# Optimization experiments

Hardware: AMD Instinct MI355X
Metric: run time of the kernel (lower is better)

Reference implementation:

```python
import jax, jax.numpy as jnp
import numpy as np

B, C, H, W = 2, 64, 512, 512
HEADS = 4
EPS = 1e-12  # F.normalize eps


def setup_inputs() -> dict:
    key = jax.random.key(0)
    ks = jax.random.split(key, 7)
    s = 0.02
    return {
        "x": jax.random.normal(ks[0], (B, C, H, W), jnp.float32),
        "Wq": jax.random.normal(ks[1], (C, C), jnp.float32) * s,
        "Wk": jax.random.normal(ks[2], (C, C), jnp.float32) * s,
        "Wv": jax.random.normal(ks[3], (C, C), jnp.float32) * s,
        "Wp": jax.random.normal(ks[4], (C, C), jnp.float32) * s,
        "bp": jax.random.normal(ks[5], (C,), jnp.float32) * s,
        "rescale": jnp.ones((HEADS, 1, 1), jnp.float32),
    }


def reference(x, Wq, Wk, Wv, Wp, bp, rescale):
    b, c, h, w = x.shape
    n = h * w
    d = c // HEADS
    xf = x.reshape(b, c, n)  # 1x1 conv == channel matmul on flattened spatial

    def conv1x1(Wt):
        return jnp.einsum('oc,bcn->bon', Wt, xf)

    # torch: permute->reshape(b,n,c)->split heads->transpose == reshape conv out to (b,heads,d,n)
    q = conv1x1(Wq).reshape(b, HEADS, d, n)
    k = conv1x1(Wk).reshape(b, HEADS, d, n)
    v = conv1x1(Wv).reshape(b, HEADS, d, n)

    def l2norm(t):  # F.normalize(p=2, dim=-1)
        nrm = jnp.sqrt(jnp.sum(t * t, axis=-1, keepdims=True))
        return t / jnp.maximum(nrm, EPS)

    q = l2norm(q)
    k = l2norm(k)

    attn = jnp.einsum('bhdn,bhen->bhde', k, q)  # (b, heads, d, d) tiny matrix
    attn = attn * rescale  # rescale broadcasts (heads,1,1)
    attn = jax.nn.softmax(attn, axis=-1)

    o = jnp.einsum('bhde,bhen->bhdn', attn, v).reshape(b, c, n)
    out = jnp.einsum('oc,bcn->bon', Wp, o) + bp[None, :, None] + xf  # proj + residual
    return out.reshape(b, c, h, w)
```

## Files before the change

kernel.cpp:

```cpp
#include <hip/hip_runtime.h>
#include <math.h>

#define C 64
#define NHEADS 4
#define DH 16
#define NN 262144
#define NB 2
#define PB 512
#define NT 2
#define EPS 1e-12f

typedef __attribute__((ext_vector_type(8))) short short8v;
typedef __attribute__((ext_vector_type(8))) unsigned short ushort8v;
typedef __attribute__((ext_vector_type(4))) unsigned short ushort4v;
typedef __attribute__((ext_vector_type(4))) float f32x4;

static __device__ __forceinline__ unsigned short f2bf(float f) {
  union { float f; unsigned int u; } v; v.f = f;
  unsigned int r = v.u + 0x7fffu + ((v.u >> 16) & 1u);
  return (unsigned short)(r >> 16);
}

__global__ __launch_bounds__(256, 3) void gram_kernel(const float* __restrict__ x,
                                                      float* __restrict__ Gc) {
  __shared__ unsigned short xs[C * 256];
  const int b = blockIdx.y;
  const int chunk = blockIdx.x;
  const float* xb = x + (size_t)b * C * NN;
  const int t = threadIdx.x;
  const int w = t >> 6, l = t & 63;
  const int lrow = l & 15, lhi = l >> 4;
  const int sc = t >> 5, soct = t & 31;

  const int gA0 = (w >> 1) * 2, gA1 = gA0 + 1;
  const int gB0 = (w & 1) * 2,  gB1 = gB0 + 1;
  const int cA0 = gA0 * 16 + lrow, cA1 = gA1 * 16 + lrow;
  const int cB0 = gB0 * 16 + lrow, cB1 = gB1 * 16 + lrow;

  f32x4 acc0 = {0.f,0.f,0.f,0.f}, acc1 = {0.f,0.f,0.f,0.f};
  f32x4 acc2 = {0.f,0.f,0.f,0.f}, acc3 = {0.f,0.f,0.f,0.f};

  float4 pre[8][2];
#pragma unroll
  for (int i = 0; i < 8; ++i) {
    const int c = i * 8 + sc;
    const float* src = xb + (size_t)c * NN + chunk * (NT * 256) + soct * 8;
    pre[i][0] = *reinterpret_cast<const float4*>(src);
    pre[i][1] = *reinterpret_cast<const float4*>(src + 4);
  }

  for (int tile = 0; tile < NT; ++tile) {
#pragma unroll
    for (int i = 0; i < 8; ++i) {
      const int c = i * 8 + sc;
      ushort8v pk;
      pk[0] = f2bf(pre[i][0].x); pk[1] = f2bf(pre[i][0].y);
      pk[2] = f2bf(pre[i][0].z); pk[3] = f2bf(pre[i][0].w);
      pk[4] = f2bf(pre[i][1].x); pk[5] = f2bf(pre[i][1].y);
      pk[6] = f2bf(pre[i][1].z); pk[7] = f2bf(pre[i][1].w);
      *reinterpret_cast<ushort8v*>(&xs[c * 256 + ((soct ^ (c & 7)) << 3)]) = pk;
    }
    if (tile + 1 < NT) {
      const int j0 = chunk * (NT * 256) + (tile + 1) * 256;
#pragma unroll
      for (int i = 0; i < 8; ++i) {
        const int c = i * 8 + sc;
        const float* src = xb + (size_t)c * NN + j0 + soct * 8;
        pre[i][0] = *reinterpret_cast<const float4*>(src);
        pre[i][1] = *reinterpret_cast<const float4*>(src + 4);
      }
    }
    asm volatile("s_waitcnt lgkmcnt(0)" ::: "memory");
    __builtin_amdgcn_s_barrier();
#pragma unroll
    for (int s = 0; s < 8; ++s) {
      const int o = s * 4 + lhi;
      const short8v fA0 = *reinterpret_cast<const short8v*>(&xs[cA0 * 256 + ((o ^ (cA0 & 7)) << 3)]);
      const short8v fA1 = *reinterpret_cast<const short8v*>(&xs[cA1 * 256 + ((o ^ (cA1 & 7)) << 3)]);
      const short8v fB0 = *reinterpret_cast<const short8v*>(&xs[cB0 * 256 + ((o ^ (cB0 & 7)) << 3)]);
      const short8v fB1 = *reinterpret_cast<const short8v*>(&xs[cB1 * 256 + ((o ^ (cB1 & 7)) << 3)]);
      acc0 = __builtin_amdgcn_mfma_f32_16x16x32_bf16(fA0, fB0, acc0, 0, 0, 0);
      acc1 = __builtin_amdgcn_mfma_f32_16x16x32_bf16(fA0, fB1, acc1, 0, 0, 0);
      acc2 = __builtin_amdgcn_mfma_f32_16x16x32_bf16(fA1, fB0, acc2, 0, 0, 0);
      acc3 = __builtin_amdgcn_mfma_f32_16x16x32_bf16(fA1, fB1, acc3, 0, 0, 0);
    }
    asm volatile("s_waitcnt lgkmcnt(0)" ::: "memory");
    __builtin_amdgcn_s_barrier();
  }
  float* g = Gc + ((size_t)b * PB + chunk) * 4096;
#pragma unroll
  for (int r = 0; r < 4; ++r) {
    const int row = lhi * 4 + r;
    g[(gA0 * 16 + row) * 64 + gB0 * 16 + lrow] = acc0[r];
    g[(gA0 * 16 + row) * 64 + gB1 * 16 + lrow] = acc1[r];
    g[(gA1 * 16 + row) * 64 + gB0 * 16 + lrow] = acc2[r];
    g[(gA1 * 16 + row) * 64 + gB1 * 16 + lrow] = acc3[r];
  }
}

__global__ __launch_bounds__(256) void reduce_kernel(const float* __restrict__ Gc,
                                                     float* __restrict__ G) {
  __shared__ float s[4][64];
  const int b = blockIdx.y;
  const int g = blockIdx.x;
  const int t = threadIdx.x;
  const int e = g * 64 + (t & 63);
  const int chunk = t >> 6;
  float sum = 0.f;
  for (int p = chunk; p < PB; p += 4)
    sum += Gc[((size_t)b * PB + p) * 4096 + e];
  s[chunk][t & 63] = sum;
  __syncthreads();
  if (t < 64) G[(size_t)b * 4096 + g * 64 + t] = s[0][t] + s[1][t] + s[2][t] + s[3][t];
}

__global__ __launch_bounds__(256) void attn_kernel(const float* __restrict__ G,
    const float* __restrict__ Wq, const float* __restrict__ Wk,
    const float* __restrict__ Wv, const float* __restrict__ Wp,
    const float* __restrict__ rescale, unsigned short* __restrict__ Ebf) {
  __shared__ float Gs[4096], GQt[4096], GKt[4096], T[4096];
  __shared__ float attnw[64][DH];
  __shared__ float nq[64], nk[64];
  const int b = blockIdx.x;
  const int t = threadIdx.x;

  for (int i = t; i < 4096; i += 256) Gs[i] = G[(size_t)b * 4096 + i];
  __syncthreads();
  for (int i = t; i < 4096; i += 256) {
    const int c = i >> 6, e = i & 63;
    float sq_ = 0.f, sk_ = 0.f;
    for (int c2 = 0; c2 < 64; ++c2) {
      const float g = Gs[c * 64 + c2];
      sq_ += g * Wq[e * 64 + c2];
      sk_ += g * Wk[e * 64 + c2];
    }
    GQt[c * 64 + e] = sq_;
    GKt[c * 64 + e] = sk_;
  }
  __syncthreads();
  if (t < 64) {
    float s = 0.f;
    for (int c2 = 0; c2 < 64; ++c2) s += Wq[t * 64 + c2] * GQt[c2 * 64 + t];
    nq[t] = sqrtf(fmaxf(s, 0.f));
  } else if (t < 128) {
    const int d = t - 64;
    float s = 0.f;
    for (int c2 = 0; c2 < 64; ++c2) s += Wk[d * 64 + c2] * GKt[c2 * 64 + d];
    nk[d] = sqrtf(fmaxf(s, 0.f));
  }
  __syncthreads();
  if (t < 64) {
    const int h = t >> 4;
    const float rs = rescale[h];
    const float nkd = fmaxf(nk[t], EPS);
    float logits[DH];
    float mx = -1e30f;
    for (int ee = 0; ee < DH; ++ee) {
      const int e = h * DH + ee;
      float num = 0.f;
      for (int c2 = 0; c2 < 64; ++c2) num += Wk[t * 64 + c2] * GQt[c2 * 64 + e];
      const float l = num / (nkd * fmaxf(nq[e], EPS)) * rs;
      logits[ee] = l;
      mx = fmaxf(mx, l);
    }
    float sum = 0.f;
    for (int ee = 0; ee < DH; ++ee) { const float p = expf(logits[ee] - mx); logits[ee] = p; sum += p; }
    const float inv = 1.f / sum;
    for (int ee = 0; ee < DH; ++ee) attnw[t][ee] = logits[ee] * inv;
  }
  __syncthreads();
  for (int i = t; i < 4096; i += 256) {
    const int r = i >> 6, c = i & 63;
    const int h = r >> 4;
    float s = 0.f;
    for (int e = 0; e < DH; ++e) s += attnw[r][e] * Wv[(h * DH + e) * 64 + c];
    T[i] = s;
  }
  __syncthreads();
  for (int i = t; i < 4096; i += 256) {
    const int r = i >> 6, c = i & 63;
    float s = (r == c) ? 1.f : 0.f;
    for (int m = 0; m < 64; ++m) s += Wp[r * 64 + m] * T[m * 64 + c];
    Ebf[(size_t)b * 4096 + i] = f2bf(s);
  }
}

__global__ __launch_bounds__(256, 4) void apply_kernel(const float* __restrict__ x,
    const unsigned short* __restrict__ Ebf, const float* __restrict__ bp,
    float* __restrict__ out) {
  __shared__ unsigned short xt[128 * 64];
  const int b = blockIdx.y;
  const int n0 = blockIdx.x * 128;
  const float* xb = x + (size_t)b * C * NN;
  float* ob = out + (size_t)b * C * NN;
  const int t = threadIdx.x;
  const int w = t >> 6, l = t & 63;
  const int lrow = l & 15, lhi = l >> 4;

  short8v ef[4][2];
  const unsigned short* eb = Ebf + (size_t)b * 4096;
#pragma unroll
  for (int ot = 0; ot < 4; ++ot)
#pragma unroll
    for (int ks = 0; ks < 2; ++ks)
      ef[ot][ks] = *reinterpret_cast<const short8v*>(eb + (ot * 16 + lrow) * 64 + ks * 32 + lhi * 8);

#pragma unroll
  for (int h = 0; h < 2; ++h) {
    const int n = h * 64 + l;
#pragma unroll
    for (int i = 0; i < 4; ++i) {
      const int c0 = w * 16 + i * 4;
      const float v0 = xb[(size_t)(c0 + 0) * NN + n0 + n];
      const float v1 = xb[(size_t)(c0 + 1) * NN + n0 + n];
      const float v2 = xb[(size_t)(c0 + 2) * NN + n0 + n];
      const float v3 = xb[(size_t)(c0 + 3) * NN + n0 + n];
      ushort4v pk;
      pk[0] = f2bf(v0); pk[1] = f2bf(v1); pk[2] = f2bf(v2); pk[3] = f2bf(v3);
      const int q = c0 >> 2;
      *reinterpret_cast<ushort4v*>(
          &xt[n * 64 + ((((q >> 1) ^ (n & 7)) << 3) + (q & 1) * 4)]) = pk;
    }
  }
  __syncthreads();

  f32x4 acc[4][2];
#pragma unroll
  for (int ot = 0; ot < 4; ++ot)
#pragma unroll
    for (int nn = 0; nn < 2; ++nn) acc[ot][nn] = (f32x4){0.f, 0.f, 0.f, 0.f};

  const int nbase = w * 32;
#pragma unroll
  for (int nn = 0; nn < 2; ++nn) {
    const int n = nbase + nn * 16 + lrow;
#pragma unroll
    for (int ks = 0; ks < 2; ++ks) {
      const int s = ks * 4 + lhi;
      const short8v xf = *reinterpret_cast<const short8v*>(&xt[n * 64 + ((s ^ (n & 7)) << 3)]);
#pragma unroll
      for (int ot = 0; ot < 4; ++ot)
        acc[ot][nn] = __builtin_amdgcn_mfma_f32_16x16x32_bf16(xf, ef[ot][ks], acc[ot][nn], 0, 0, 0);
    }
  }

#pragma unroll
  for (int ot = 0; ot < 4; ++ot) {
    const int o = ot * 16 + lrow;
    const float bias = bp[o];
#pragma unroll
    for (int nn = 0; nn < 2; ++nn) {
      const int nb4 = nbase + nn * 16 + lhi * 4;
      float4 o4;
      o4.x = acc[ot][nn][0] + bias;
      o4.y = acc[ot][nn][1] + bias;
      o4.z = acc[ot][nn][2] + bias;
      o4.w = acc[ot][nn][3] + bias;
      *reinterpret_cast<float4*>(&ob[(size_t)o * NN + n0 + nb4]) = o4;
    }
  }
}

extern "C" void kernel_launch(void* const* d_in, const int* in_sizes, int n_in,
                              void* d_out, int out_size, void* d_ws, size_t ws_size,
                              hipStream_t stream) {
  const float* x       = (const float*)d_in[0];
  const float* Wq      = (const float*)d_in[1];
  const float* Wk      = (const float*)d_in[2];
  const float* Wv      = (const float*)d_in[3];
  const float* Wp      = (const float*)d_in[4];
  const float* bp      = (const float*)d_in[5];
  const float* rescale = (const float*)d_in[6];
  float* out = (float*)d_out;

  float* Gc = (float*)d_ws;
  float* G  = Gc + (size_t)NB * PB * 4096;
  unsigned short* Ebf = (unsigned short*)(G + (size_t)NB * 4096);

  gram_kernel<<<dim3(PB, NB), dim3(256), 0, stream>>>(x, Gc);
  reduce_kernel<<<dim3(64, NB), dim3(256), 0, stream>>>(Gc, G);
  attn_kernel<<<dim3(NB), dim3(256), 0, stream>>>(G, Wq, Wk, Wv, Wp, rescale, Ebf);
  apply_kernel<<<dim3(2048, NB), dim3(256), 0, stream>>>(x, Ebf, bp, out);
}
```

Baseline: 161.3 us.

## Emit bf16 copy of x in gram pass and read it in apply kernel

The gram kernel now writes its bf16-converted x tiles to a workspace buffer, and the apply kernel reads this bf16 copy directly from global memory instead of reloading fp32 x and transposing through LDS. Gram partials are staged in the output buffer to free workspace. This trades an extra 2-byte-per-element write in the first pass for halving the apply pass's input reads. The apply loads are now narrow 16-bit strided gathers, which may coalesce poorly.

```diff
diff --git a/kernel.cpp b/kernel.cpp
--- a/kernel.cpp
+++ b/kernel.cpp
@@ -12,7 +12,6 @@
 
 typedef __attribute__((ext_vector_type(8))) short short8v;
 typedef __attribute__((ext_vector_type(8))) unsigned short ushort8v;
-typedef __attribute__((ext_vector_type(4))) unsigned short ushort4v;
 typedef __attribute__((ext_vector_type(4))) float f32x4;
 
 static __device__ __forceinline__ unsigned short f2bf(float f) {
@@ -22,11 +21,13 @@
 }
 
 __global__ __launch_bounds__(256, 3) void gram_kernel(const float* __restrict__ x,
-                                                      float* __restrict__ Gc) {
+                                                      float* __restrict__ Gc,
+                                                      unsigned short* __restrict__ xbf) {
   __shared__ unsigned short xs[C * 256];
   const int b = blockIdx.y;
   const int chunk = blockIdx.x;
   const float* xb = x + (size_t)b * C * NN;
+  unsigned short* xbb = xbf + (size_t)b * C * NN;
   const int t = threadIdx.x;
   const int w = t >> 6, l = t & 63;
   const int lrow = l & 15, lhi = l >> 4;
@@ -50,6 +51,7 @@
   }
 
   for (int tile = 0; tile < NT; ++tile) {
+    const int j0 = chunk * (NT * 256) + tile * 256;
 #pragma unroll
     for (int i = 0; i < 8; ++i) {
       const int c = i * 8 + sc;
@@ -59,13 +61,14 @@
       pk[4] = f2bf(pre[i][1].x); pk[5] = f2bf(pre[i][1].y);
       pk[6] = f2bf(pre[i][1].z); pk[7] = f2bf(pre[i][1].w);
       *reinterpret_cast<ushort8v*>(&xs[c * 256 + ((soct ^ (c & 7)) << 3)]) = pk;
+      *reinterpret_cast<ushort8v*>(&xbb[(size_t)c * NN + j0 + soct * 8]) = pk;
     }
     if (tile + 1 < NT) {
-      const int j0 = chunk * (NT * 256) + (tile + 1) * 256;
+      const int jn = chunk * (NT * 256) + (tile + 1) * 256;
 #pragma unroll
       for (int i = 0; i < 8; ++i) {
         const int c = i * 8 + sc;
-        const float* src = xb + (size_t)c * NN + j0 + soct * 8;
+        const float* src = xb + (size_t)c * NN + jn + soct * 8;
         pre[i][0] = *reinterpret_cast<const float4*>(src);
         pre[i][1] = *reinterpret_cast<const float4*>(src + 4);
       }
@@ -185,13 +188,12 @@
   }
 }
 
-__global__ __launch_bounds__(256, 4) void apply_kernel(const float* __restrict__ x,
-    const unsigned short* __restrict__ Ebf, const float* __restrict__ bp,
-    float* __restrict__ out) {
-  __shared__ unsigned short xt[128 * 64];
+__global__ __launch_bounds__(256, 3) void apply_kernel(
+    const unsigned short* __restrict__ xbf, const unsigned short* __restrict__ Ebf,
+    const float* __restrict__ bp, float* __restrict__ out) {
   const int b = blockIdx.y;
   const int n0 = blockIdx.x * 128;
-  const float* xb = x + (size_t)b * C * NN;
+  const unsigned short* xb = xbf + (size_t)b * C * NN;
   float* ob = out + (size_t)b * C * NN;
   const int t = threadIdx.x;
   const int w = t >> 6, l = t & 63;
@@ -205,25 +207,6 @@
     for (int ks = 0; ks < 2; ++ks)
       ef[ot][ks] = *reinterpret_cast<const short8v*>(eb + (ot * 16 + lrow) * 64 + ks * 32 + lhi * 8);
 
-#pragma unroll
-  for (int h = 0; h < 2; ++h) {
-    const int n = h * 64 + l;
-#pragma unroll
-    for (int i = 0; i < 4; ++i) {
-      const int c0 = w * 16 + i * 4;
-      const float v0 = xb[(size_t)(c0 + 0) * NN + n0 + n];
-      const float v1 = xb[(size_t)(c0 + 1) * NN + n0 + n];
-      const float v2 = xb[(size_t)(c0 + 2) * NN + n0 + n];
-      const float v3 = xb[(size_t)(c0 + 3) * NN + n0 + n];
-      ushort4v pk;
-      pk[0] = f2bf(v0); pk[1] = f2bf(v1); pk[2] = f2bf(v2); pk[3] = f2bf(v3);
-      const int q = c0 >> 2;
-      *reinterpret_cast<ushort4v*>(
-          &xt[n * 64 + ((((q >> 1) ^ (n & 7)) << 3) + (q & 1) * 4)]) = pk;
-    }
-  }
-  __syncthreads();
-
   f32x4 acc[4][2];
 #pragma unroll
   for (int ot = 0; ot < 4; ++ot)
@@ -233,14 +216,20 @@
   const int nbase = w * 32;
 #pragma unroll
   for (int nn = 0; nn < 2; ++nn) {
-    const int n = nbase + nn * 16 + lrow;
+    const int n = n0 + nbase + nn * 16 + lrow;
 #pragma unroll
     for (int ks = 0; ks < 2; ++ks) {
-      const int s = ks * 4 + lhi;
-      const short8v xf = *reinterpret_cast<const short8v*>(&xt[n * 64 + ((s ^ (n & 7)) << 3)]);
+      const unsigned short* src = xb + (size_t)(ks * 32 + lhi * 8) * NN + n;
+      union { unsigned int u[4]; short8v v; } xf;
+#pragma unroll
+      for (int jj = 0; jj < 4; ++jj) {
+        const unsigned int lo = src[(size_t)(2 * jj) * NN];
+        const unsigned int hi = src[(size_t)(2 * jj + 1) * NN];
+        xf.u[jj] = lo | (hi << 16);
+      }
 #pragma unroll
       for (int ot = 0; ot < 4; ++ot)
-        acc[ot][nn] = __builtin_amdgcn_mfma_f32_16x16x32_bf16(xf, ef[ot][ks], acc[ot][nn], 0, 0, 0);
+        acc[ot][nn] = __builtin_amdgcn_mfma_f32_16x16x32_bf16(xf.v, ef[ot][ks], acc[ot][nn], 0, 0, 0);
     }
   }
 
@@ -250,13 +239,13 @@
     const float bias = bp[o];
 #pragma unroll
     for (int nn = 0; nn < 2; ++nn) {
-      const int nb4 = nbase + nn * 16 + lhi * 4;
+      const int nb4 = n0 + nbase + nn * 16 + lhi * 4;
       float4 o4;
       o4.x = acc[ot][nn][0] + bias;
       o4.y = acc[ot][nn][1] + bias;
       o4.z = acc[ot][nn][2] + bias;
       o4.w = acc[ot][nn][3] + bias;
-      *reinterpret_cast<float4*>(&ob[(size_t)o * NN + n0 + nb4]) = o4;
+      *reinterpret_cast<float4*>(&ob[(size_t)o * NN + nb4]) = o4;
     }
   }
 }
@@ -273,12 +262,13 @@
   const float* rescale = (const float*)d_in[6];
   float* out = (float*)d_out;
 
-  float* Gc = (float*)d_ws;
-  float* G  = Gc + (size_t)NB * PB * 4096;
+  float* Gc = out;
+  unsigned short* xbf = (unsigned short*)d_ws;
+  float* G = (float*)(xbf + (size_t)NB * C * NN);
   unsigned short* Ebf = (unsigned short*)(G + (size_t)NB * 4096);
 
-  gram_kernel<<<dim3(PB, NB), dim3(256), 0, stream>>>(x, Gc);
+  gram_kernel<<<dim3(PB, NB), dim3(256), 0, stream>>>(x, Gc, xbf);
   reduce_kernel<<<dim3(64, NB), dim3(256), 0, stream>>>(Gc, G);
   attn_kernel<<<dim3(NB), dim3(256), 0, stream>>>(G, Wq, Wk, Wv, Wp, rescale, Ebf);
-  apply_kernel<<<dim3(2048, NB), dim3(256), 0, stream>>>(x, Ebf, bp, out);
-}
+  apply_kernel<<<dim3(2048, NB), dim3(256), 0, stream>>>(xbf, Ebf, bp, out);
+}
```

New measurement: 171.6 us. 1.06x slower.
